# Performance work log

Hardware: AMD Instinct MI355X
Metric: run time of the kernel (lower is better)

The kernel has to match this reference:

```python
import jax, jax.numpy as jnp
import numpy as np

B, L, KDIM, QDIM, ADIM, ODIM, H = 4, 1024, 1024, 1024, 1024, 1024, 16
DK = ADIM // H
SCALE = float(np.sqrt(DK))
NEG_INF = float(np.finfo(np.float32).min)


def setup_inputs() -> dict:
    key = jax.random.key(0)
    ks = jax.random.split(key, 12)
    s = 0.02
    return {
        "key": jax.random.normal(ks[0], (B, L, KDIM), jnp.float32),
        "value": jax.random.normal(ks[1], (B, L, KDIM), jnp.float32),
        "query": jax.random.normal(ks[2], (B, L, QDIM), jnp.float32),
        "mask": jax.random.randint(ks[3], (B, L, L), 0, 2, jnp.int32),
        "Wk": jax.random.normal(ks[4], (ADIM, KDIM), jnp.float32) * s,
        "bk": jnp.zeros((ADIM,), jnp.float32),
        "Wv": jax.random.normal(ks[5], (ADIM, KDIM), jnp.float32) * s,
        "bv": jnp.zeros((ADIM,), jnp.float32),
        "Wq": jax.random.normal(ks[6], (ADIM, QDIM), jnp.float32) * s,
        "bq": jnp.zeros((ADIM,), jnp.float32),
        "Wo": jax.random.normal(ks[7], (ODIM, ADIM), jnp.float32) * s,
        "bo": jnp.zeros((ODIM,), jnp.float32),
    }


def reference(key, value, query, mask, Wk, bk, Wv, bv, Wq, bq, Wo, bo):
    bs, klen = key.shape[0], key.shape[1]
    qlen = query.shape[1]
    # projections -> [B, len, H, d_k]
    k = (key @ Wk.T + bk).reshape(bs, klen, H, DK)
    v = (value @ Wv.T + bv).reshape(bs, klen, H, DK)
    q = (query @ Wq.T + bq).reshape(bs, qlen, H, DK)
    # attention energy [B, qlen, klen, H]
    e = jnp.einsum('bihd,bjhd->bijh', q, k) / SCALE
    m = mask[:, :, :, None]  # [B,q,k,1] broadcasts over heads
    e = jnp.where(m == 0, NEG_INF, e)
    aw = jax.nn.softmax(e, axis=2)  # softmax over klen
    cv = jnp.einsum('bijh,bjhd->bihd', aw, v).reshape(bs, qlen, ADIM)
    cv = cv @ Wo.T + bo
    return cv, jnp.transpose(aw, (0, 3, 1, 2))  # [B,H,q,k]
```

## Files before the change

### kernel.cpp

```cpp
#include <hip/hip_runtime.h>
#include <hip/hip_bf16.h>

typedef __attribute__((ext_vector_type(8))) __bf16 bf16x8;
typedef __attribute__((ext_vector_type(8))) short short8;
typedef __attribute__((ext_vector_type(4))) short s16x4;
typedef __attribute__((ext_vector_type(4))) float f32x4;

#define LN 1024
#define NH 16
#define DKH 64

__device__ __forceinline__ short f2bf(float f) {
    unsigned u = __builtin_bit_cast(unsigned, f);
    u = u + 0x7fffu + ((u >> 16) & 1u);
    return (short)(u >> 16);
}
__device__ __forceinline__ float bf2f(short s) {
    return __builtin_bit_cast(float, ((unsigned)(unsigned short)s) << 16);
}

__device__ __forceinline__ void gl_lds16(const short* g, short* l) {
    __builtin_amdgcn_global_load_lds(
        (const __attribute__((address_space(1))) void*)g,
        (__attribute__((address_space(3))) void*)l, 16, 0, 0);
}

__global__ __launch_bounds__(256) void prep_all(
    const float* __restrict__ q, const float* __restrict__ k, const float* __restrict__ v,
    const float* __restrict__ wq, const float* __restrict__ wk,
    const float* __restrict__ wv, const float* __restrict__ wo,
    short* __restrict__ dq, short* __restrict__ dk, short* __restrict__ dv,
    short* __restrict__ dwq, short* __restrict__ dwk,
    short* __restrict__ dwv, short* __restrict__ dwo,
    const int* __restrict__ mask, unsigned long long* __restrict__ bits)
{
    int bid = blockIdx.x;
    if (bid < 8192) {
        const float* s; short* d; int base;
        if      (bid < 2048) { s = q;  d = dq;  base = bid; }
        else if (bid < 4096) { s = k;  d = dk;  base = bid - 2048; }
        else if (bid < 6144) { s = v;  d = dv;  base = bid - 4096; }
        else if (bid < 6656) { s = wq; d = dwq; base = bid - 6144; }
        else if (bid < 7168) { s = wk; d = dwk; base = bid - 6656; }
        else if (bid < 7680) { s = wv; d = dwv; base = bid - 7168; }
        else                 { s = wo; d = dwo; base = bid - 7680; }
        int i = base * 256 + threadIdx.x;
        f32x4 a = ((const f32x4*)s)[i * 2];
        f32x4 b = ((const f32x4*)s)[i * 2 + 1];
        short8 o;
        #pragma unroll
        for (int j = 0; j < 4; ++j) { o[j] = f2bf(a[j]); o[4 + j] = f2bf(b[j]); }
        ((short8*)d)[i] = o;
    } else {
        int mid = bid - 8192;
        const int i = mid & 1023;
        const int b = mid >> 10;
        const int qq = threadIdx.x >> 6;
        const int lane = threadIdx.x & 63;
        const int* mp = &mask[((size_t)b * LN + i) * LN + qq * 256 + lane * 4];
        int4 mv = *(const int4*)mp;
        unsigned long long b0 = __ballot(mv.x != 0);
        unsigned long long b1 = __ballot(mv.y != 0);
        unsigned long long b2 = __ballot(mv.z != 0);
        unsigned long long b3 = __ballot(mv.w != 0);
        if (lane == 0) {
            unsigned long long* o = &bits[(((size_t)b * LN + i) * 4 + qq) * 4];
            o[0] = b0; o[1] = b1; o[2] = b2; o[3] = b3;
        }
    }
}

template<int MODE>
__device__ __forceinline__ void gemm_body(
    const short* __restrict__ A, const short* __restrict__ Bt,
    const float* __restrict__ bias, void* __restrict__ Cp,
    int m0, int n0, int N, int K, short* lA, short* lB)
{
    const int tid = threadIdx.x;
    const int lane = tid & 63;
    const int wid = tid >> 6;
    const int wr = wid >> 1, wc = wid & 1;
    const int lr = lane & 15, lg = lane >> 4;

    int srow[2], skc[2];
    #pragma unroll
    for (int p = 0; p < 2; ++p) {
        int ch = p * 256 + wid * 64 + lane;
        srow[p] = ch >> 3;
        skc[p] = (((ch & 7) ^ (srow[p] & 7))) * 8;
    }

    f32x4 acc[2][2] = {};

    for (int k0 = 0; k0 < K; k0 += 64) {
        #pragma unroll
        for (int p = 0; p < 2; ++p) {
            short* dstA = &lA[(p * 256 + wid * 64) * 8];
            short* dstB = &lB[(p * 256 + wid * 64) * 8];
            gl_lds16(A  + (size_t)(m0 + srow[p]) * K + k0 + skc[p], dstA);
            gl_lds16(Bt + (size_t)(n0 + srow[p]) * K + k0 + skc[p], dstB);
        }
        __syncthreads();
        bf16x8 af[2][2], bfr[2][2];
        #pragma unroll
        for (int kh = 0; kh < 2; ++kh) {
            #pragma unroll
            for (int m = 0; m < 2; ++m) {
                int arow = wr * 32 + m * 16 + lr;
                af[kh][m] = *(const bf16x8*)&lA[arow * 64 + (((kh * 4 + lg) ^ (arow & 7)) * 8)];
            }
            #pragma unroll
            for (int n = 0; n < 2; ++n) {
                int brow = wc * 32 + n * 16 + lr;
                bfr[kh][n] = *(const bf16x8*)&lB[brow * 64 + (((kh * 4 + lg) ^ (brow & 7)) * 8)];
            }
        }
        #pragma unroll
        for (int kh = 0; kh < 2; ++kh)
            #pragma unroll
            for (int m = 0; m < 2; ++m)
                #pragma unroll
                for (int n = 0; n < 2; ++n)
                    acc[m][n] = __builtin_amdgcn_mfma_f32_16x16x32_bf16(af[kh][m], bfr[kh][n], acc[m][n], 0, 0, 0);
        __syncthreads();
    }

    #pragma unroll
    for (int m = 0; m < 2; ++m)
        #pragma unroll
        for (int n = 0; n < 2; ++n) {
            int col = n0 + wc * 32 + n * 16 + lr;
            float bb = bias[col];
            if (MODE == 1) {
                int row = m0 + wr * 32 + m * 16 + lg * 4;
                int bb_i = row >> 10, tok = row & 1023;
                int hh = col >> 6, dd = col & 63;
                s16x4 o;
                #pragma unroll
                for (int r = 0; r < 4; ++r) o[r] = f2bf(acc[m][n][r] + bb);
                *(s16x4*)&((short*)Cp)[((size_t)((bb_i * NH + hh) * DKH) + dd) * LN + tok] = o;
            } else {
                #pragma unroll
                for (int r = 0; r < 4; ++r) {
                    int row = m0 + wr * 32 + m * 16 + lg * 4 + r;
                    float v = acc[m][n][r] + bb;
                    if (MODE == 2) ((float*)Cp)[(size_t)row * N + col] = v;
                    else           ((short*)Cp)[(size_t)row * N + col] = f2bf(v);
                }
            }
        }
}

__global__ __launch_bounds__(256) void gemm_vq(
    const short* __restrict__ vin, const short* __restrict__ qin,
    const short* __restrict__ wv, const short* __restrict__ wq,
    const float* __restrict__ bv, const float* __restrict__ bq,
    short* __restrict__ vT, short* __restrict__ q_bf)
{
    __shared__ short lA[64 * 64];
    __shared__ short lB[64 * 64];
    const int m0 = blockIdx.y * 64, n0 = blockIdx.x * 64;
    if (blockIdx.z == 0)
        gemm_body<1>(vin, wv, bv, vT, m0, n0, 1024, 1024, lA, lB);
    else
        gemm_body<0>(qin, wq, bq, q_bf, m0, n0, 1024, 1024, lA, lB);
}

__global__ __launch_bounds__(256) void gemm_bf(
    const short* __restrict__ A, const short* __restrict__ Bt,
    const float* __restrict__ bias, short* __restrict__ C)
{
    __shared__ short lA[64 * 64];
    __shared__ short lB[64 * 64];
    gemm_body<0>(A, Bt, bias, C, blockIdx.y * 64, blockIdx.x * 64, 1024, 1024, lA, lB);
}

__global__ __launch_bounds__(256) void gemm_out(
    const short* __restrict__ A, const short* __restrict__ Bt,
    const float* __restrict__ bias, float* __restrict__ C)
{
    __shared__ short lA[64 * 64];
    __shared__ short lB[64 * 64];
    gemm_body<2>(A, Bt, bias, C, blockIdx.y * 64, blockIdx.x * 64, 1024, 1024, lA, lB);
}

__global__ __launch_bounds__(256, 2) void attn_kernel(
    const short* __restrict__ qb, const short* __restrict__ kb,
    const short* __restrict__ vT, const unsigned long long* __restrict__ mb,
    float* __restrict__ aw, short* __restrict__ cv)
{
    __shared__ short p_lds[32 * 1024];
    __shared__ float redbuf[4][32];

    const int bid = blockIdx.x;
    const int swz = (bid & 7) * 256 + (bid >> 3);
    const int i0 = (swz & 31) * 32;
    const int h = (swz >> 5) & 15;
    const int b = swz >> 9;

    const int tid = threadIdx.x;
    const int lane = tid & 63;
    const int w = tid >> 6;
    const int lr = lane & 15, lg = lane >> 4;

    unsigned long long Bm[2][4];
    #pragma unroll
    for (int g = 0; g < 2; ++g)
        #pragma unroll
        for (int r = 0; r < 4; ++r)
            Bm[g][r] = mb[(((size_t)b * LN + i0 + g * 16 + lg * 4 + r) * 4 + w) * 4 + (lr & 3)] >> (lr >> 2);

    bf16x8 a0[2], a1[2];
    #pragma unroll
    for (int g = 0; g < 2; ++g) {
        const short* qp = &qb[((size_t)b * LN + i0 + g * 16 + lr) * 1024 + h * 64 + lg * 8];
        a0[g] = *(const bf16x8*)qp;
        a1[g] = *(const bf16x8*)(qp + 32);
    }

    f32x4 acc[2][16];
    #pragma unroll
    for (int g = 0; g < 2; ++g)
        #pragma unroll
        for (int jf = 0; jf < 16; ++jf) acc[g][jf] = f32x4{0.f, 0.f, 0.f, 0.f};

    const size_t krow_base = (size_t)b * LN;
    #pragma unroll
    for (int jf = 0; jf < 16; ++jf) {
        int j0f = w * 256 + jf * 16;
        const short* kp = &kb[(krow_base + j0f + lr) * 1024 + h * 64 + lg * 8];
        bf16x8 b0 = *(const bf16x8*)kp;
        bf16x8 b1 = *(const bf16x8*)(kp + 32);
        acc[0][jf] = __builtin_amdgcn_mfma_f32_16x16x32_bf16(a0[0], b0, acc[0][jf], 0, 0, 0);
        acc[0][jf] = __builtin_amdgcn_mfma_f32_16x16x32_bf16(a1[0], b1, acc[0][jf], 0, 0, 0);
        acc[1][jf] = __builtin_amdgcn_mfma_f32_16x16x32_bf16(a0[1], b0, acc[1][jf], 0, 0, 0);
        acc[1][jf] = __builtin_amdgcn_mfma_f32_16x16x32_bf16(a1[1], b1, acc[1][jf], 0, 0, 0);
    }

    float ps[2][4] = {};
    #pragma unroll
    for (int g = 0; g < 2; ++g)
        #pragma unroll
        for (int jf = 0; jf < 16; ++jf)
            #pragma unroll
            for (int r = 0; r < 4; ++r) {
                float p = ((Bm[g][r] >> (jf * 4)) & 1ULL) ? __expf(acc[g][jf][r] * 0.125f) : 0.0f;
                acc[g][jf][r] = p;
                ps[g][r] += p;
            }

    #pragma unroll
    for (int g = 0; g < 2; ++g)
        #pragma unroll
        for (int r = 0; r < 4; ++r) {
            for (int off = 1; off < 16; off <<= 1) ps[g][r] += __shfl_xor(ps[g][r], off, 64);
        }
    if (lr == 0) {
        #pragma unroll
        for (int g = 0; g < 2; ++g)
            #pragma unroll
            for (int r = 0; r < 4; ++r) redbuf[w][g * 16 + lg * 4 + r] = ps[g][r];
    }

    #pragma unroll
    for (int g = 0; g < 2; ++g)
        #pragma unroll
        for (int jf = 0; jf < 16; ++jf) {
            int j = w * 256 + jf * 16 + lr;
            #pragma unroll
            for (int r = 0; r < 4; ++r) {
                int row = g * 16 + lg * 4 + r;
                int byte = (row * 2048 + j * 2) ^ ((row & 7) << 4);
                *(short*)((char*)p_lds + byte) = f2bf(acc[g][jf][r]);
            }
        }
    __syncthreads();

    f32x4 accA[2] = {}, accB[2] = {};
    const int d0 = w * 16;
    const short* vrow = vT + ((size_t)((b * NH + h) * DKH) + d0 + lr) * LN;
    #pragma unroll
    for (int ks = 0; ks < 32; ks += 2) {
        bf16x8 vb0 = *(const bf16x8*)&vrow[ks * 32 + lg * 8];
        bf16x8 vb1 = *(const bf16x8*)&vrow[(ks + 1) * 32 + lg * 8];
        #pragma unroll
        for (int g = 0; g < 2; ++g) {
            int row = g * 16 + lr;
            int byte0 = (row * 2048 + (ks * 32 + lg * 8) * 2) ^ ((row & 7) << 4);
            int byte1 = (row * 2048 + ((ks + 1) * 32 + lg * 8) * 2) ^ ((row & 7) << 4);
            bf16x8 pa0 = *(const bf16x8*)((char*)p_lds + byte0);
            bf16x8 pa1 = *(const bf16x8*)((char*)p_lds + byte1);
            accA[g] = __builtin_amdgcn_mfma_f32_16x16x32_bf16(pa0, vb0, accA[g], 0, 0, 0);
            accB[g] = __builtin_amdgcn_mfma_f32_16x16x32_bf16(pa1, vb1, accB[g], 0, 0, 0);
        }
    }

    float inv[2][4];
    #pragma unroll
    for (int g = 0; g < 2; ++g)
        #pragma unroll
        for (int r = 0; r < 4; ++r) {
            float s = redbuf[0][g * 16 + lg * 4 + r];
            for (int ww = 1; ww < 4; ++ww) s += redbuf[ww][g * 16 + lg * 4 + r];
            inv[g][r] = 1.0f / s;
        }
    #pragma unroll
    for (int g = 0; g < 2; ++g)
        #pragma unroll
        for (int r = 0; r < 4; ++r) {
            int irow = i0 + g * 16 + lg * 4 + r;
            cv[((size_t)b * LN + irow) * 1024 + h * 64 + d0 + lr] = f2bf((accA[g][r] + accB[g][r]) * inv[g][r]);
        }

    {
        const int arow = tid >> 3;
        const int ac0 = tid & 7;
        float s = redbuf[0][arow] + redbuf[1][arow] + redbuf[2][arow] + redbuf[3][arow];
        float ainv = 1.0f / s;
        float* awr = aw + ((size_t)(b * NH + h) * LN + i0 + arow) * LN;
        const int abase = arow * 2048;
        const int aswz = (arow & 7) << 4;
        #pragma unroll
        for (int it = 0; it < 16; ++it) {
            int k = ac0 + it * 8;
            int byte = (abase + k * 16) ^ aswz;
            short8 pv = *(const short8*)((char*)p_lds + byte);
            f32x4 o0, o1;
            #pragma unroll
            for (int j = 0; j < 4; ++j) {
                o0[j] = bf2f(pv[j]) * ainv;
                o1[j] = bf2f(pv[4 + j]) * ainv;
            }
            *(f32x4*)&awr[k * 8] = o0;
            *(f32x4*)&awr[k * 8 + 4] = o1;
        }
    }
}

extern "C" void kernel_launch(void* const* d_in, const int* in_sizes, int n_in,
                              void* d_out, int out_size, void* d_ws, size_t ws_size,
                              hipStream_t stream) {
    (void)in_sizes; (void)n_in; (void)out_size; (void)ws_size;
    const float* key   = (const float*)d_in[0];
    const float* value = (const float*)d_in[1];
    const float* query = (const float*)d_in[2];
    const int*   mask  = (const int*)d_in[3];
    const float* Wk = (const float*)d_in[4];
    const float* bk = (const float*)d_in[5];
    const float* Wv = (const float*)d_in[6];
    const float* bv = (const float*)d_in[7];
    const float* Wq = (const float*)d_in[8];
    const float* bq = (const float*)d_in[9];
    const float* Wo = (const float*)d_in[10];
    const float* bo = (const float*)d_in[11];

    float* out_cv = (float*)d_out;
    float* out_aw = out_cv + (size_t)4096 * 1024;

    unsigned long long* mbits_g = (unsigned long long*)out_cv;
    short* q_bf = (short*)((char*)d_out + (size_t)(1u << 19));

    const size_t MB = 1u << 20;
    char* ws = (char*)d_ws;
    short* qin  = (short*)(ws + 0 * MB);   short* k_bf  = qin;
    short* kin  = (short*)(ws + 8 * MB);   short* cv_bf = kin;
    short* vin  = (short*)(ws + 16 * MB);
    short* wq   = (short*)(ws + 24 * MB);
    short* wk   = (short*)(ws + 26 * MB);
    short* wv   = (short*)(ws + 28 * MB);
    short* wo   = (short*)(ws + 30 * MB);
    short* vT   = (short*)(ws + 32 * MB);

    dim3 blk(256);
    prep_all<<<dim3(12288), blk, 0, stream>>>(
        query, key, value, Wq, Wk, Wv, Wo,
        qin, kin, vin, wq, wk, wv, wo,
        mask, mbits_g);

    gemm_vq<<<dim3(16, 64, 2), blk, 0, stream>>>(vin, qin, wv, wq, bv, bq, vT, q_bf);
    gemm_bf<<<dim3(16, 64), blk, 0, stream>>>(kin, wk, bk, k_bf);
    attn_kernel<<<dim3(2048), blk, 0, stream>>>(q_bf, k_bf, vT, mbits_g, out_aw, cv_bf);
    gemm_out<<<dim3(16, 64), blk, 0, stream>>>(cv_bf, wo, bo, out_cv);
}
```

Baseline: 203.0 us.

## Fuse Q/K/V projections into one launch with 128x128 GEMM tiles

Adds a 128x128-tile GEMM body with a 4x4 MFMA accumulator per wave and one kernel that computes the V, Q and K projections across three z-slices. When the workspace is large enough, K gets its own buffer so it no longer aliases the query input. This removes a launch and raises operand reuse per LDS load. In exchange there are fewer blocks (768), more registers and more LDS per block, and the old path stays as a fallback.

```diff
diff --git a/kernel.cpp b/kernel.cpp
--- a/kernel.cpp
+++ b/kernel.cpp
@@ -95,10 +95,8 @@
     for (int k0 = 0; k0 < K; k0 += 64) {
         #pragma unroll
         for (int p = 0; p < 2; ++p) {
-            short* dstA = &lA[(p * 256 + wid * 64) * 8];
-            short* dstB = &lB[(p * 256 + wid * 64) * 8];
-            gl_lds16(A  + (size_t)(m0 + srow[p]) * K + k0 + skc[p], dstA);
-            gl_lds16(Bt + (size_t)(n0 + srow[p]) * K + k0 + skc[p], dstB);
+            gl_lds16(A  + (size_t)(m0 + srow[p]) * K + k0 + skc[p], &lA[(p * 256 + wid * 64) * 8]);
+            gl_lds16(Bt + (size_t)(n0 + srow[p]) * K + k0 + skc[p], &lB[(p * 256 + wid * 64) * 8]);
         }
         __syncthreads();
         bf16x8 af[2][2], bfr[2][2];
@@ -149,6 +147,100 @@
                 }
             }
         }
+}
+
+template<int MODE>
+__device__ __forceinline__ void gemm_body128(
+    const short* __restrict__ A, const short* __restrict__ Bt,
+    const float* __restrict__ bias, void* __restrict__ Cp,
+    int m0, int n0, int N, int K, short* lA, short* lB)
+{
+    const int tid = threadIdx.x;
+    const int lane = tid & 63;
+    const int wid = tid >> 6;
+    const int wr = wid >> 1, wc = wid & 1;
+    const int lr = lane & 15, lg = lane >> 4;
+
+    int srow[4], skc[4];
+    #pragma unroll
+    for (int p = 0; p < 4; ++p) {
+        int ch = p * 256 + wid * 64 + lane;
+        srow[p] = ch >> 3;
+        skc[p] = (((ch & 7) ^ (srow[p] & 7))) * 8;
+    }
+
+    f32x4 acc[4][4] = {};
+
+    for (int k0 = 0; k0 < K; k0 += 64) {
+        #pragma unroll
+        for (int p = 0; p < 4; ++p) {
+            gl_lds16(A  + (size_t)(m0 + srow[p]) * K + k0 + skc[p], &lA[(p * 256 + wid * 64) * 8]);
+            gl_lds16(Bt + (size_t)(n0 + srow[p]) * K + k0 + skc[p], &lB[(p * 256 + wid * 64) * 8]);
+        }
+        __syncthreads();
+        #pragma unroll
+        for (int kh = 0; kh < 2; ++kh) {
+            bf16x8 af[4], bfr[4];
+            #pragma unroll
+            for (int m = 0; m < 4; ++m) {
+                int arow = wr * 64 + m * 16 + lr;
+                af[m] = *(const bf16x8*)&lA[arow * 64 + (((kh * 4 + lg) ^ (arow & 7)) * 8)];
+            }
+            #pragma unroll
+            for (int n = 0; n < 4; ++n) {
+                int brow = wc * 64 + n * 16 + lr;
+                bfr[n] = *(const bf16x8*)&lB[brow * 64 + (((kh * 4 + lg) ^ (brow & 7)) * 8)];
+            }
+            #pragma unroll
+            for (int m = 0; m < 4; ++m)
+                #pragma unroll
+                for (int n = 0; n < 4; ++n)
+                    acc[m][n] = __builtin_amdgcn_mfma_f32_16x16x32_bf16(af[m], bfr[n], acc[m][n], 0, 0, 0);
+        }
+        __syncthreads();
+    }
+
+    #pragma unroll
+    for (int m = 0; m < 4; ++m)
+        #pragma unroll
+        for (int n = 0; n < 4; ++n) {
+            int col = n0 + wc * 64 + n * 16 + lr;
+            float bb = bias[col];
+            if (MODE == 1) {
+                int row = m0 + wr * 64 + m * 16 + lg * 4;
+                int bb_i = row >> 10, tok = row & 1023;
+                int hh = col >> 6, dd = col & 63;
+                s16x4 o;
+                #pragma unroll
+                for (int r = 0; r < 4; ++r) o[r] = f2bf(acc[m][n][r] + bb);
+                *(s16x4*)&((short*)Cp)[((size_t)((bb_i * NH + hh) * DKH) + dd) * LN + tok] = o;
+            } else {
+                #pragma unroll
+                for (int r = 0; r < 4; ++r) {
+                    int row = m0 + wr * 64 + m * 16 + lg * 4 + r;
+                    float v = acc[m][n][r] + bb;
+                    if (MODE == 2) ((float*)Cp)[(size_t)row * N + col] = v;
+                    else           ((short*)Cp)[(size_t)row * N + col] = f2bf(v);
+                }
+            }
+        }
+}
+
+__global__ __launch_bounds__(256) void gemm_qkv128(
+    const short* __restrict__ vin, const short* __restrict__ qin, const short* __restrict__ kin,
+    const short* __restrict__ wv, const short* __restrict__ wq, const short* __restrict__ wk,
+    const float* __restrict__ bv, const float* __restrict__ bq, const float* __restrict__ bk,
+    short* __restrict__ vT, short* __restrict__ q_bf, short* __restrict__ k_bf)
+{
+    __shared__ short lA[128 * 64];
+    __shared__ short lB[128 * 64];
+    const int m0 = blockIdx.y * 128, n0 = blockIdx.x * 128;
+    if (blockIdx.z == 0)
+        gemm_body128<1>(vin, wv, bv, vT, m0, n0, 1024, 1024, lA, lB);
+    else if (blockIdx.z == 1)
+        gemm_body128<0>(qin, wq, bq, q_bf, m0, n0, 1024, 1024, lA, lB);
+    else
+        gemm_body128<0>(kin, wk, bk, k_bf, m0, n0, 1024, 1024, lA, lB);
 }
 
 __global__ __launch_bounds__(256) void gemm_vq(
@@ -340,7 +432,7 @@
 extern "C" void kernel_launch(void* const* d_in, const int* in_sizes, int n_in,
                               void* d_out, int out_size, void* d_ws, size_t ws_size,
                               hipStream_t stream) {
-    (void)in_sizes; (void)n_in; (void)out_size; (void)ws_size;
+    (void)in_sizes; (void)n_in; (void)out_size;
     const float* key   = (const float*)d_in[0];
     const float* value = (const float*)d_in[1];
     const float* query = (const float*)d_in[2];
@@ -362,7 +454,7 @@
 
     const size_t MB = 1u << 20;
     char* ws = (char*)d_ws;
-    short* qin  = (short*)(ws + 0 * MB);   short* k_bf  = qin;
+    short* qin  = (short*)(ws + 0 * MB);
     short* kin  = (short*)(ws + 8 * MB);   short* cv_bf = kin;
     short* vin  = (short*)(ws + 16 * MB);
     short* wq   = (short*)(ws + 24 * MB);
@@ -377,8 +469,16 @@
         qin, kin, vin, wq, wk, wv, wo,
         mask, mbits_g);
 
-    gemm_vq<<<dim3(16, 64, 2), blk, 0, stream>>>(vin, qin, wv, wq, bv, bq, vT, q_bf);
-    gemm_bf<<<dim3(16, 64), blk, 0, stream>>>(kin, wk, bk, k_bf);
-    attn_kernel<<<dim3(2048), blk, 0, stream>>>(q_bf, k_bf, vT, mbits_g, out_aw, cv_bf);
+    if (ws_size >= (size_t)48 * MB) {
+        short* k_bf = (short*)(ws + 40 * MB);
+        gemm_qkv128<<<dim3(8, 32, 3), blk, 0, stream>>>(
+            vin, qin, kin, wv, wq, wk, bv, bq, bk, vT, q_bf, k_bf);
+        attn_kernel<<<dim3(2048), blk, 0, stream>>>(q_bf, k_bf, vT, mbits_g, out_aw, cv_bf);
+    } else {
+        short* k_bf = qin;
+        gemm_vq<<<dim3(16, 64, 2), blk, 0, stream>>>(vin, qin, wv, wq, bv, bq, vT, q_bf);
+        gemm_bf<<<dim3(16, 64), blk, 0, stream>>>(kin, wk, bk, k_bf);
+        attn_kernel<<<dim3(2048), blk, 0, stream>>>(q_bf, k_bf, vT, mbits_g, out_aw, cv_bf);
+    }
     gemm_out<<<dim3(16, 64), blk, 0, stream>>>(cv_bf, wo, bo, out_cv);
 }
```

New measurement: 198.6 us (median of 2 runs). -2.2%, faster.
